# Performance work log

Hardware: AMD Instinct MI355X
Metric: run time of the kernel (lower is better)

Reference implementation:

```python
import jax, jax.numpy as jnp
import numpy as np

N, IN, OUT, E, S = 65536, 512, 512, 8, 64


def setup_inputs() -> dict:
    key = jax.random.key(0)
    k1, k2, k3, k4, k5 = jax.random.split(key, 5)
    bound = float(np.sqrt(1.0 / IN))
    x = jax.random.normal(k1, (N, IN), dtype=jnp.float32)
    expert_coefficients = jax.random.normal(k2, (S, E), dtype=jnp.float32)
    batch_indices = jax.random.randint(k3, (N,), 0, S)
    weights = jax.random.uniform(k4, (E, OUT, IN), dtype=jnp.float32, minval=-bound, maxval=bound)
    bias = jax.random.uniform(k5, (OUT,), dtype=jnp.float32, minval=-bound, maxval=bound)
    return {"x": x, "expert_coefficients": expert_coefficients,
            "batch_indices": batch_indices, "weights": weights, "bias": bias}


def reference(x, expert_coefficients, batch_indices, weights, bias):
    # Original computes mixed_weights[b] = sum_e coeff[b,e] * W[e], then for each
    # system b applies mixed_weights[b] to the atoms with batch_indices == b via a
    # masked scan. Linearity lets us equivalently gather per-atom expert
    # coefficients and contract once, avoiding the O(num_systems * N) waste:
    #   out[n,o] = sum_e coeff[batch_indices[n], e] * sum_i W[e,o,i] * x[n,i]
    coeff_per_atom = expert_coefficients[batch_indices]  # [N, E]
    out = jnp.einsum('ni,eoi,ne->no', x, weights, coeff_per_atom)  # [N, OUT]
    return out + bias
```

## Files before the change

kernel.cpp:

```cpp
#include <hip/hip_runtime.h>
#include <hip/hip_bf16.h>

#define NA   65536
#define DIN  512
#define DOUT 512
#define NE   8
#define NS   64
#define CAP  2048
#define BM   128
#define BN   128
#define BK   32

typedef __attribute__((ext_vector_type(8))) __bf16 bf16x8;
typedef __attribute__((ext_vector_type(4))) __bf16 bf16x4;
typedef __attribute__((ext_vector_type(4))) float floatx4;

__device__ __forceinline__ void async_load16(const void* g, void* l) {
  __builtin_amdgcn_global_load_lds(
      (__attribute__((address_space(1))) void*)(void*)g,
      (__attribute__((address_space(3))) void*)l,
      16, 0, 0);
}

__global__ void init_kernel(int* cursors) {
  int t = threadIdx.x;
  if (t < NS) cursors[t] = t * CAP;
}

__global__ void scatter_kernel(const int* __restrict__ bidx,
                               int* __restrict__ cursors,
                               int* __restrict__ perm) {
  __shared__ int hist[NS];
  __shared__ int base[NS];
  int t = threadIdx.x;
  if (t < NS) hist[t] = 0;
  __syncthreads();
  int n = blockIdx.x * 256 + t;
  int s = bidx[n];
  int rank = atomicAdd(&hist[s], 1);
  __syncthreads();
  if (t < NS && hist[t] > 0) base[t] = atomicAdd(&cursors[t], hist[t]);
  __syncthreads();
  perm[base[s] + rank] = n;
}

__global__ void mixw_kernel(const float* __restrict__ W,
                            const float* __restrict__ coeff,
                            ushort* __restrict__ mixedW) {
  int t = threadIdx.x;
  int base = blockIdx.x * 2048 + t * 8;
  float w[NE][8];
#pragma unroll
  for (int e = 0; e < NE; e++) {
    const float4* p = (const float4*)(W + e * (DOUT * DIN) + base);
    float4 a = p[0], b = p[1];
    w[e][0] = a.x; w[e][1] = a.y; w[e][2] = a.z; w[e][3] = a.w;
    w[e][4] = b.x; w[e][5] = b.y; w[e][6] = b.z; w[e][7] = b.w;
  }
  int s0 = blockIdx.y * 32;
  for (int si = 0; si < 32; si++) {
    int s = s0 + si;
    float o[8] = {0, 0, 0, 0, 0, 0, 0, 0};
#pragma unroll
    for (int e = 0; e < NE; e++) {
      float c = coeff[s * NE + e];
#pragma unroll
      for (int j = 0; j < 8; j++) o[j] += c * w[e][j];
    }
    union { bf16x8 v; uint4 u; } cv;
#pragma unroll
    for (int j = 0; j < 8; j++) cv.v[j] = (__bf16)o[j];
    *(uint4*)(mixedW + (size_t)s * (DOUT * DIN) + base) = cv.u;
  }
}

__global__ __launch_bounds__(256) void gemm_kernel(
    const float* __restrict__ x, const ushort* __restrict__ mixedW,
    const int* __restrict__ perm, const int* __restrict__ cursors,
    const float* __restrict__ bias, float* __restrict__ out) {
  int st = blockIdx.y;
  int s = st >> 4;
  int tt = st & 15;
  int count = cursors[s] - s * CAP;
  int r0 = tt * BM;
  if (r0 >= count) return;
  int rows = min(BM, count - r0);
  int n0 = blockIdx.x * BN;

  __shared__ __align__(16) ushort Alds[BM * BK];
  __shared__ __align__(16) ushort Blds[BN * BK];
  __shared__ int prow[BM];

  int tid = threadIdx.x;
  int lane = tid & 63;
  int wave = tid >> 6;

  if (tid < BM) prow[tid] = perm[s * CAP + r0 + min(tid, rows - 1)];
  __syncthreads();

  int chunk = tid & 7;
  const float* aptr[4];
#pragma unroll
  for (int q = 0; q < 4; q++) {
    int row = q * 32 + (tid >> 3);
    aptr[q] = x + (size_t)prow[row] * DIN + chunk * 4;
  }
  const ushort* bptr[2];
  ushort* bl[2];
#pragma unroll
  for (int j = 0; j < 2; j++) {
    int region = j * 4 + wave;
    int row = region * 16 + (lane >> 2);
    bptr[j] = mixedW + (size_t)s * (DOUT * DIN) + (size_t)(n0 + row) * DIN +
              (lane & 3) * 8;
    bl[j] = Blds + region * 512;
  }

  floatx4 acc[4][4];
#pragma unroll
  for (int mt = 0; mt < 4; mt++)
#pragma unroll
    for (int nt = 0; nt < 4; nt++) acc[mt][nt] = {0.f, 0.f, 0.f, 0.f};

  int wm = wave >> 1, wn = wave & 1;
  int m15 = lane & 15, quad = lane >> 4;

  for (int kk = 0; kk < DIN; kk += BK) {
#pragma unroll
    for (int j = 0; j < 2; j++) async_load16(bptr[j] + kk, bl[j]);
#pragma unroll
    for (int q = 0; q < 4; q++) {
      float4 v = *(const float4*)(aptr[q] + kk);
      bf16x4 h;
      h[0] = (__bf16)v.x; h[1] = (__bf16)v.y;
      h[2] = (__bf16)v.z; h[3] = (__bf16)v.w;
      int row = q * 32 + (tid >> 3);
      *(bf16x4*)(Alds + row * BK + chunk * 4) = h;
    }
    __syncthreads();
    bf16x8 af[4], bfm[4];
#pragma unroll
    for (int i = 0; i < 4; i++) {
      af[i]  = *(const bf16x8*)(Alds + (wm * 64 + i * 16 + m15) * BK + quad * 8);
      bfm[i] = *(const bf16x8*)(Blds + (wn * 64 + i * 16 + m15) * BK + quad * 8);
    }
#pragma unroll
    for (int mt = 0; mt < 4; mt++)
#pragma unroll
      for (int nt = 0; nt < 4; nt++)
        acc[mt][nt] = __builtin_amdgcn_mfma_f32_16x16x32_bf16(
            af[mt], bfm[nt], acc[mt][nt], 0, 0, 0);
    __syncthreads();
  }

  float bv[4];
#pragma unroll
  for (int nt = 0; nt < 4; nt++) bv[nt] = bias[n0 + wn * 64 + nt * 16 + m15];

#pragma unroll
  for (int mt = 0; mt < 4; mt++) {
    int rb = wm * 64 + mt * 16 + quad * 4;
    int pr[4];
#pragma unroll
    for (int r = 0; r < 4; r++) pr[r] = prow[rb + r];
#pragma unroll
    for (int nt = 0; nt < 4; nt++) {
      int col = n0 + wn * 64 + nt * 16 + m15;
#pragma unroll
      for (int r = 0; r < 4; r++) {
        if (rb + r < rows)
          out[(size_t)pr[r] * DOUT + col] = acc[mt][nt][r] + bv[nt];
      }
    }
  }
}

extern "C" void kernel_launch(void* const* d_in, const int* in_sizes, int n_in,
                              void* d_out, int out_size, void* d_ws,
                              size_t ws_size, hipStream_t stream) {
  const float* x     = (const float*)d_in[0];
  const float* coeff = (const float*)d_in[1];
  const int*   bidx  = (const int*)d_in[2];
  const float* W     = (const float*)d_in[3];
  const float* bias  = (const float*)d_in[4];
  float* out = (float*)d_out;

  char* ws = (char*)d_ws;
  int* cursors   = (int*)ws;
  int* perm      = (int*)(ws + 1024);
  ushort* mixedW = (ushort*)(ws + 1024 + CAP * NS * sizeof(int));

  hipLaunchKernelGGL(init_kernel, dim3(1), dim3(64), 0, stream, cursors);
  hipLaunchKernelGGL(scatter_kernel, dim3(NA / 256), dim3(256), 0, stream,
                     bidx, cursors, perm);
  hipLaunchKernelGGL(mixw_kernel, dim3(DOUT * DIN / 2048, 2), dim3(256), 0,
                     stream, W, coeff, mixedW);
  hipLaunchKernelGGL(gemm_kernel, dim3(DOUT / BN, NS * 16), dim3(256), 0,
                     stream, x, mixedW, perm, cursors, bias, out);
}
```

Baseline: 368.2 us.

## Stream fp32 A tiles asynchronously into LDS, compact perm via count+scan, widen mixw grid

The A operand (gathered rows of x) is now loaded as fp32 directly into LDS with global_load_lds, instead of going through registers and converting to bf16 before the LDS store. The bf16 conversion moves to the fragment read from LDS. The LDS layout of both A and B changes to a k-chunk-major arrangement. Per-system slots are now laid out compactly using a count kernel and a serial scan in place of fixed CAP slots, and mixw_kernel gets 8 blocks along y instead of 2 for more parallelism. The trade-off is double the A LDS footprint, two extra small kernel launches, and a conversion repeated per wave on the read side.

```diff
diff --git a/kernel.cpp b/kernel.cpp
--- a/kernel.cpp
+++ b/kernel.cpp
@@ -6,13 +6,12 @@
 #define DOUT 512
 #define NE   8
 #define NS   64
-#define CAP  2048
 #define BM   128
 #define BN   128
 #define BK   32
+#define TPS  16
 
 typedef __attribute__((ext_vector_type(8))) __bf16 bf16x8;
-typedef __attribute__((ext_vector_type(4))) __bf16 bf16x4;
 typedef __attribute__((ext_vector_type(4))) float floatx4;
 
 __device__ __forceinline__ void async_load16(const void* g, void* l) {
@@ -22,9 +21,34 @@
       16, 0, 0);
 }
 
-__global__ void init_kernel(int* cursors) {
-  int t = threadIdx.x;
-  if (t < NS) cursors[t] = t * CAP;
+__global__ void init_kernel(int* counts) {
+  int t = threadIdx.x;
+  if (t < NS) counts[t] = 0;
+}
+
+__global__ void count_kernel(const int* __restrict__ bidx,
+                             int* __restrict__ counts) {
+  __shared__ int hist[NS];
+  int t = threadIdx.x;
+  if (t < NS) hist[t] = 0;
+  __syncthreads();
+  int s = bidx[blockIdx.x * 256 + t];
+  atomicAdd(&hist[s], 1);
+  __syncthreads();
+  if (t < NS && hist[t] > 0) atomicAdd(&counts[t], hist[t]);
+}
+
+__global__ void scan_kernel(const int* __restrict__ counts,
+                            int* __restrict__ starts,
+                            int* __restrict__ cursors) {
+  if (threadIdx.x == 0) {
+    int run = 0;
+    for (int s = 0; s < NS; s++) {
+      starts[s] = run;
+      cursors[s] = run;
+      run += counts[s];
+    }
+  }
 }
 
 __global__ void scatter_kernel(const int* __restrict__ bidx,
@@ -57,8 +81,8 @@
     w[e][0] = a.x; w[e][1] = a.y; w[e][2] = a.z; w[e][3] = a.w;
     w[e][4] = b.x; w[e][5] = b.y; w[e][6] = b.z; w[e][7] = b.w;
   }
-  int s0 = blockIdx.y * 32;
-  for (int si = 0; si < 32; si++) {
+  int s0 = blockIdx.y * 8;
+  for (int si = 0; si < 8; si++) {
     int s = s0 + si;
     float o[8] = {0, 0, 0, 0, 0, 0, 0, 0};
 #pragma unroll
@@ -76,18 +100,20 @@
 
 __global__ __launch_bounds__(256) void gemm_kernel(
     const float* __restrict__ x, const ushort* __restrict__ mixedW,
-    const int* __restrict__ perm, const int* __restrict__ cursors,
-    const float* __restrict__ bias, float* __restrict__ out) {
+    const int* __restrict__ perm, const int* __restrict__ starts,
+    const int* __restrict__ counts, const float* __restrict__ bias,
+    float* __restrict__ out) {
   int st = blockIdx.y;
   int s = st >> 4;
   int tt = st & 15;
-  int count = cursors[s] - s * CAP;
+  int count = counts[s];
   int r0 = tt * BM;
   if (r0 >= count) return;
   int rows = min(BM, count - r0);
   int n0 = blockIdx.x * BN;
-
-  __shared__ __align__(16) ushort Alds[BM * BK];
+  int base = starts[s] + r0;
+
+  __shared__ __align__(16) float  Alds[BM * BK];
   __shared__ __align__(16) ushort Blds[BN * BK];
   __shared__ int prow[BM];
 
@@ -95,25 +121,22 @@
   int lane = tid & 63;
   int wave = tid >> 6;
 
-  if (tid < BM) prow[tid] = perm[s * CAP + r0 + min(tid, rows - 1)];
-  __syncthreads();
-
-  int chunk = tid & 7;
+  if (tid < BM) prow[tid] = perm[base + min(tid, rows - 1)];
+  __syncthreads();
+
   const float* aptr[4];
 #pragma unroll
-  for (int q = 0; q < 4; q++) {
-    int row = q * 32 + (tid >> 3);
-    aptr[q] = x + (size_t)prow[row] * DIN + chunk * 4;
+  for (int j = 0; j < 4; j++) {
+    int L = j * 256 + tid;
+    int row = L & 127, c = L >> 7;
+    aptr[j] = x + (size_t)prow[row] * DIN + c * 4;
   }
   const ushort* bptr[2];
-  ushort* bl[2];
 #pragma unroll
   for (int j = 0; j < 2; j++) {
-    int region = j * 4 + wave;
-    int row = region * 16 + (lane >> 2);
-    bptr[j] = mixedW + (size_t)s * (DOUT * DIN) + (size_t)(n0 + row) * DIN +
-              (lane & 3) * 8;
-    bl[j] = Blds + region * 512;
+    int L = j * 256 + tid;
+    int col = L & 127, c = L >> 7;
+    bptr[j] = mixedW + (size_t)s * (DOUT * DIN) + (size_t)(n0 + col) * DIN + c * 8;
   }
 
   floatx4 acc[4][4];
@@ -127,22 +150,27 @@
 
   for (int kk = 0; kk < DIN; kk += BK) {
 #pragma unroll
-    for (int j = 0; j < 2; j++) async_load16(bptr[j] + kk, bl[j]);
-#pragma unroll
-    for (int q = 0; q < 4; q++) {
-      float4 v = *(const float4*)(aptr[q] + kk);
-      bf16x4 h;
-      h[0] = (__bf16)v.x; h[1] = (__bf16)v.y;
-      h[2] = (__bf16)v.z; h[3] = (__bf16)v.w;
-      int row = q * 32 + (tid >> 3);
-      *(bf16x4*)(Alds + row * BK + chunk * 4) = h;
-    }
+    for (int j = 0; j < 4; j++)
+      async_load16(aptr[j] + kk, (char*)Alds + j * 4096 + wave * 1024);
+#pragma unroll
+    for (int j = 0; j < 2; j++)
+      async_load16(bptr[j] + kk, (char*)Blds + j * 4096 + wave * 1024);
     __syncthreads();
+
     bf16x8 af[4], bfm[4];
 #pragma unroll
     for (int i = 0; i < 4; i++) {
-      af[i]  = *(const bf16x8*)(Alds + (wm * 64 + i * 16 + m15) * BK + quad * 8);
-      bfm[i] = *(const bf16x8*)(Blds + (wn * 64 + i * 16 + m15) * BK + quad * 8);
+      int row = wm * 64 + i * 16 + m15;
+      floatx4 lo = *(const floatx4*)(Alds + (2 * quad) * 512 + row * 4);
+      floatx4 hi = *(const floatx4*)(Alds + (2 * quad + 1) * 512 + row * 4);
+      bf16x8 h;
+      h[0] = (__bf16)lo[0]; h[1] = (__bf16)lo[1];
+      h[2] = (__bf16)lo[2]; h[3] = (__bf16)lo[3];
+      h[4] = (__bf16)hi[0]; h[5] = (__bf16)hi[1];
+      h[6] = (__bf16)hi[2]; h[7] = (__bf16)hi[3];
+      af[i] = h;
+      int col = wn * 64 + i * 16 + m15;
+      bfm[i] = *(const bf16x8*)(Blds + quad * 1024 + col * 8);
     }
 #pragma unroll
     for (int mt = 0; mt < 4; mt++)
@@ -186,15 +214,21 @@
   float* out = (float*)d_out;
 
   char* ws = (char*)d_ws;
-  int* cursors   = (int*)ws;
-  int* perm      = (int*)(ws + 1024);
-  ushort* mixedW = (ushort*)(ws + 1024 + CAP * NS * sizeof(int));
-
-  hipLaunchKernelGGL(init_kernel, dim3(1), dim3(64), 0, stream, cursors);
+  int* counts  = (int*)ws;
+  int* starts  = (int*)(ws + 256);
+  int* cursors = (int*)(ws + 512);
+  int* perm    = (int*)(ws + 1024);
+  ushort* mixedW = (ushort*)(ws + 1024 + NA * sizeof(int));
+
+  hipLaunchKernelGGL(init_kernel, dim3(1), dim3(64), 0, stream, counts);
+  hipLaunchKernelGGL(count_kernel, dim3(NA / 256), dim3(256), 0, stream,
+                     bidx, counts);
+  hipLaunchKernelGGL(scan_kernel, dim3(1), dim3(64), 0, stream,
+                     counts, starts, cursors);
   hipLaunchKernelGGL(scatter_kernel, dim3(NA / 256), dim3(256), 0, stream,
                      bidx, cursors, perm);
-  hipLaunchKernelGGL(mixw_kernel, dim3(DOUT * DIN / 2048, 2), dim3(256), 0,
+  hipLaunchKernelGGL(mixw_kernel, dim3(DOUT * DIN / 2048, 8), dim3(256), 0,
                      stream, W, coeff, mixedW);
-  hipLaunchKernelGGL(gemm_kernel, dim3(DOUT / BN, NS * 16), dim3(256), 0,
-                     stream, x, mixedW, perm, cursors, bias, out);
-}
+  hipLaunchKernelGGL(gemm_kernel, dim3(DOUT / BN, NS * TPS), dim3(256), 0,
+                     stream, x, mixedW, perm, starts, counts, bias, out);
+}
```

Result: slower. 433.5 us (+17.7%).
